# Optimization experiments

Measured on AMD Instinct MI355X. Metric: run time of the kernel, lower is better.

## Reference

```python
import jax, jax.numpy as jnp
from jax import lax
import numpy as np

B, CIN, COUT, H, W = 8, 64, 64, 128, 128
K = 3
KK = K * K  # 9 kernel taps


def setup_inputs() -> dict:
    key = jax.random.key(0)
    ks = jax.random.split(key, 10)
    n = jax.random.normal
    s = 0.05  # keep activations in a sane range
    return {
        "Fi": n(ks[0], (B, CIN, H, W), jnp.float32),
        "Fe": n(ks[1], (B, CIN, H, W), jnp.float32),
        "w1": n(ks[2], (CIN, 2 * CIN, 5, 5), jnp.float32) * s,
        "b1": n(ks[3], (CIN,), jnp.float32) * s,
        "w2": n(ks[4], (CIN, CIN, 3, 3), jnp.float32) * s,
        "b2": n(ks[5], (CIN,), jnp.float32) * s,
        "w_off": n(ks[6], (3 * KK, CIN, 3, 3), jnp.float32) * s,
        "b_off": n(ks[7], (3 * KK,), jnp.float32) * s,
        "w_dcn": n(ks[8], (COUT, CIN, 3, 3), jnp.float32) * s,
        "b_dcn": n(ks[9], (COUT,), jnp.float32) * s,
    }


def _conv(x, w, b, pad):
    y = lax.conv_general_dilated(x, w, (1, 1), [(pad, pad), (pad, pad)],
                                 dimension_numbers=('NCHW', 'OIHW', 'NCHW'))
    return y + b[None, :, None, None]


def _leaky(x):
    return jnp.where(x >= 0, x, 0.1 * x)  # LeakyReLU(0.1)


def _bilinear(img, y, x):
    # img [B,C,H,W]; y, x [B,KK,H,W] fractional sampling coords; zero padding OOB
    Bn, C, Hi, Wi = img.shape
    y0 = jnp.floor(y)
    x0 = jnp.floor(x)
    flat = img.reshape(Bn, C, Hi * Wi)
    out = jnp.zeros((Bn, C) + y.shape[1:], img.dtype)
    for dy, dx in ((0, 0), (0, 1), (1, 0), (1, 1)):
        yi = y0 + dy
        xi = x0 + dx
        wgt = (1.0 - jnp.abs(y - yi)) * (1.0 - jnp.abs(x - xi))
        valid = (yi >= 0) & (yi <= Hi - 1) & (xi >= 0) & (xi <= Wi - 1)
        yc = jnp.clip(yi, 0, Hi - 1).astype(jnp.int32)
        xc = jnp.clip(xi, 0, Wi - 1).astype(jnp.int32)
        idx = (yc * Wi + xc).reshape(Bn, 1, -1)
        v = jnp.take_along_axis(flat, jnp.broadcast_to(idx, (Bn, C, idx.shape[-1])), axis=2)
        v = v.reshape(Bn, C, *y.shape[1:])  # [B,C,KK,H,W]
        out = out + v * (wgt * valid)[:, None]
    return out


def _dcn(x, feat, w_off, b_off, w, b):
    # modulated deformable conv (DCNv2), k=3, stride=1, pad=1, dilation=1
    oo = _conv(feat, w_off, b_off, 1)                 # [B, 3*KK, H, W]
    o1, o2, m = jnp.split(oo, 3, axis=1)              # dy, dx, mask logits
    offset_out = jnp.concatenate([o1, o2], axis=1)
    mask = jax.nn.sigmoid(m)                          # [B,KK,H,W]
    ky, kx = jnp.meshgrid(jnp.arange(K), jnp.arange(K), indexing='ij')
    ky = ky.reshape(KK)
    kx = kx.reshape(KK)
    base_y = (jnp.arange(H)[None, :, None] - 1 + ky[:, None, None]).astype(x.dtype)  # [KK,H,1]
    base_x = (jnp.arange(W)[None, None, :] - 1 + kx[:, None, None]).astype(x.dtype)  # [KK,1,W]
    ys = base_y[None] + o1                            # [B,KK,H,W]
    xs = base_x[None] + o2                            # [B,KK,H,W]
    samp = _bilinear(x, ys, xs) * mask[:, None]       # [B,C,KK,H,W]
    out = jnp.einsum('bckhw,ock->bohw', samp, w.reshape(w.shape[0], w.shape[1], KK))
    return offset_out, out + b[None, :, None, None]


def reference(Fi, Fe, w1, b1, w2, b2, w_off, b_off, w_dcn, b_dcn):
    feat = _leaky(_conv(jnp.concatenate([Fi, Fe], axis=1), w1, b1, 2))
    feat = _leaky(_conv(feat, w2, b2, 1))
    offset_out, aligned = _dcn(Fe, feat, w_off, b_off, w_dcn, b_dcn)
    Ff = jnp.concatenate([Fi, aligned], axis=1)
    return offset_out, Ff
```

## Files before the change

kernel.cpp:

```cpp
#include <hip/hip_runtime.h>
#include <hip/hip_bf16.h>

typedef __bf16 bf16_t;
typedef __attribute__((ext_vector_type(8))) __bf16 bf16x8;
typedef __attribute__((ext_vector_type(4))) float f32x4;

#define Bn 8
#define Hh 128
#define Ww 128
#define HW 16384

#define WP1_B   ((size_t)0)
#define WP2_B   ((size_t)409600)
#define WPO_B   ((size_t)483328)
#define WDCN_B  ((size_t)520192)
#define BIAS_B  ((size_t)667648)
#define XT_B    ((size_t)668672)
#define F1_B    (XT_B + 33554432)
#define F2_B    (F1_B + 16777216)

__global__ void prep_kernel(const float* __restrict__ w1, const float* __restrict__ w2,
                            const float* __restrict__ woff, const float* __restrict__ wdcn,
                            const float* __restrict__ b1, const float* __restrict__ b2,
                            const float* __restrict__ boff, const float* __restrict__ bdcn,
                            char* __restrict__ wsb) {
    bf16_t* wp1 = (bf16_t*)(wsb + WP1_B);
    bf16_t* wp2 = (bf16_t*)(wsb + WP2_B);
    bf16_t* wpo = (bf16_t*)(wsb + WPO_B);
    bf16_t* wd  = (bf16_t*)(wsb + WDCN_B);
    float*  bias= (float*)(wsb + BIAS_B);
    int tid = blockIdx.x * blockDim.x + threadIdx.x;
    int nt  = gridDim.x * blockDim.x;
    for (int i = tid; i < 25*4*4*64*8; i += nt) {
        int j = i & 7, q = i >> 3;
        int n = q % 64; q /= 64;
        int g = q & 3;  q >>= 2;
        int ck = q & 3; int t = q >> 2;
        int cin = ck*32 + g*8 + j;
        wp1[i] = (bf16_t)w1[(n*128 + cin)*25 + t];
    }
    for (int i = tid; i < 9*2*4*64*8; i += nt) {
        int j = i & 7, q = i >> 3;
        int n = q % 64; q /= 64;
        int g = q & 3;  q >>= 2;
        int ck = q & 1; int t = q >> 1;
        int cin = ck*32 + g*8 + j;
        wp2[i] = (bf16_t)w2[(n*64 + cin)*9 + t];
    }
    for (int i = tid; i < 9*2*4*32*8; i += nt) {
        int j = i & 7, q = i >> 3;
        int n = q & 31; q >>= 5;
        int g = q & 3;  q >>= 2;
        int ck = q & 1; int t = q >> 1;
        int cin = ck*32 + g*8 + j;
        wpo[i] = (n < 27) ? (bf16_t)woff[(n*64 + cin)*9 + t] : (bf16_t)0.f;
    }
    for (int i = tid; i < 18*4*4*16*8; i += nt) {
        int j = i & 7, f = i >> 3;
        int l15 = f & 15; f >>= 4;
        int l4  = f & 3;  f >>= 2;
        int ntl = f & 3;  int kc = f >> 2;
        int kg = kc*32 + l4*8 + j;
        int tap = kg >> 6, c = kg & 63;
        int n = ntl*16 + l15;
        wd[i] = (bf16_t)wdcn[n*576 + c*9 + tap];
    }
    if (tid < 64) { bias[tid] = b1[tid]; bias[64+tid] = b2[tid]; bias[160+tid] = bdcn[tid]; }
    if (tid >= 64 && tid < 96) { int n = tid - 64; bias[128+n] = (n < 27) ? boff[n] : 0.f; }
}

__global__ __launch_bounds__(256) void nhwc_kernel(const float* __restrict__ Fi,
                                                   const float* __restrict__ Fe,
                                                   bf16_t* __restrict__ Xt) {
    __shared__ bf16_t tile[64][136];
    const int b  = blockIdx.y;
    const int p0 = blockIdx.x * 64;
    const int px = threadIdx.x & 63;
    const int csub = threadIdx.x >> 6;
    for (int ci = 0; ci < 32; ++ci) {
        int c = csub * 32 + ci;
        const float* src = (c < 64) ? (Fi + (((size_t)(b*64 + c)) << 14))
                                    : (Fe + (((size_t)(b*64 + (c-64))) << 14));
        tile[px][c] = (bf16_t)src[p0 + px];
    }
    __syncthreads();
    const int px2 = threadIdx.x >> 2;
    const int cc  = (threadIdx.x & 3) * 32;
    bf16x8* dst = (bf16x8*)(Xt + ((size_t)(b*HW) + p0 + px2) * 128 + cc);
    const bf16x8* srcl = (const bf16x8*)(&tile[px2][cc]);
    dst[0] = srcl[0]; dst[1] = srcl[1]; dst[2] = srcl[2]; dst[3] = srcl[3];
}

template <int CIN_, int KS, int COUTP, bool LEAKY, bool OUTF32, bool OFFS>
__global__ __launch_bounds__(256) void conv_mfma(const bf16_t* __restrict__ Xt,
                                                 const bf16_t* __restrict__ Wp,
                                                 const float* __restrict__ bias,
                                                 bf16_t* __restrict__ outb,
                                                 float* __restrict__ outf,
                                                 float* __restrict__ out0) {
    constexpr int PAD = KS / 2;
    constexpr int HR  = 4 + KS - 1;
    constexpr int HC  = 64 + KS - 1;
    constexpr int NC  = CIN_ / 32;
    constexpr int NT  = COUTP / 16;
    __shared__ bf16_t stg[HR * HC * 40];

    const int tid  = threadIdx.x;
    const int lane = tid & 63;
    const int wid  = tid >> 6;
    const int b    = blockIdx.z;
    const int h0   = blockIdx.y * 4;
    const int w0   = blockIdx.x * 64;
    const int l15  = lane & 15;
    const int l4   = lane >> 4;

    f32x4 acc[4][NT];
#pragma unroll
    for (int m = 0; m < 4; ++m)
#pragma unroll
        for (int nt = 0; nt < NT; ++nt)
#pragma unroll
            for (int r = 0; r < 4; ++r) acc[m][nt][r] = 0.f;

    const bf16_t Z0 = (bf16_t)0.f;
    const bf16x8 zv = {Z0, Z0, Z0, Z0, Z0, Z0, Z0, Z0};
    const bf16x8* wpt = (const bf16x8*)Wp;

    for (int ck = 0; ck < NC; ++ck) {
        for (int s = tid; s < HR * HC; s += 256) {
            const int srow = s / HC, scol = s % HC;
            const int gh = h0 - PAD + srow, gw = w0 - PAD + scol;
            bf16x8 v0 = zv, v1 = zv, v2 = zv, v3 = zv;
            if (((unsigned)gh < 128u) && ((unsigned)gw < 128u)) {
                const bf16x8* gp = (const bf16x8*)(Xt + (((size_t)(b*HW) + (gh << 7) + gw)) * CIN_ + ck * 32);
                v0 = gp[0]; v1 = gp[1]; v2 = gp[2]; v3 = gp[3];
            }
            bf16x8* ldst = (bf16x8*)(&stg[s * 40]);
            ldst[0] = v0; ldst[1] = v1; ldst[2] = v2; ldst[3] = v3;
        }
        __syncthreads();
        int t = 0;
#pragma unroll
        for (int dy = 0; dy < KS; ++dy) {
#pragma unroll
            for (int dx = 0; dx < KS; ++dx, ++t) {
                bf16x8 a[4];
#pragma unroll
                for (int m = 0; m < 4; ++m)
                    a[m] = *(const bf16x8*)(&stg[((wid + dy) * HC + (m * 16 + l15 + dx)) * 40 + l4 * 8]);
                bf16x8 bb[NT];
#pragma unroll
                for (int nt = 0; nt < NT; ++nt)
                    bb[nt] = wpt[((size_t)((t * NC + ck) * 4 + l4)) * COUTP + nt * 16 + l15];
#pragma unroll
                for (int m = 0; m < 4; ++m)
#pragma unroll
                    for (int nt = 0; nt < NT; ++nt)
                        acc[m][nt] = __builtin_amdgcn_mfma_f32_16x16x32_bf16(a[m], bb[nt], acc[m][nt], 0, 0, 0);
            }
        }
        __syncthreads();
    }

    const int hrow = h0 + wid;
#pragma unroll
    for (int m = 0; m < 4; ++m) {
#pragma unroll
        for (int nt = 0; nt < NT; ++nt) {
            const int n = nt * 16 + l15;
            const float bs = bias[n];
#pragma unroll
            for (int r = 0; r < 4; ++r) {
                const int px = w0 + m * 16 + l4 * 4 + r;
                float v = acc[m][nt][r] + bs;
                if (LEAKY) v = (v >= 0.f) ? v : 0.1f * v;
                const size_t pix = (size_t)(hrow << 7) + px;
                if (OUTF32) outf[(((size_t)(b * COUTP + n)) << 14) + pix] = v;
                else        outb[(((size_t)(b * HW)) + pix) * COUTP + n] = (bf16_t)v;
                if (OFFS) {
                    if (n < 18) out0[(((size_t)(b * 18 + n)) << 14) + pix] = v;
                }
            }
        }
    }
}

__global__ void copy_fi(const float* __restrict__ Fi, float* __restrict__ out1) {
    const int b = blockIdx.y;
    const int i = blockIdx.x * blockDim.x + threadIdx.x;
    const int e = i << 2;
    const int c = e >> 14;
    const int p = e & 16383;
    const float4* src = reinterpret_cast<const float4*>(Fi);
    float4* dst = reinterpret_cast<float4*>(out1);
    size_t se = ((size_t)b << 20) + e;
    size_t de = (((size_t)(b * 128 + c)) << 14) + p;
    dst[de >> 2] = src[se >> 2];
}

__global__ __launch_bounds__(512) void dcn_mfma(const bf16_t* __restrict__ Xt,
                                                const float* __restrict__ OO,
                                                const bf16_t* __restrict__ Wd,
                                                const float* __restrict__ bias,
                                                float* __restrict__ out1) {
    __shared__ bf16_t Bs[10 * 4 * 4 * 16 * 8];

    const int tid  = threadIdx.x;
    const int lane = tid & 63;
    const int wave = tid >> 6;
    const int l15  = lane & 15;
    const int l4   = lane >> 4;
    const int b    = blockIdx.y;
    const int p0   = blockIdx.x * 256 + wave * 32;

    f32x4 acc[2][4];
#pragma unroll
    for (int nt = 0; nt < 4; ++nt) {
        const float bs = bias[nt * 16 + l15];
#pragma unroll
        for (int a = 0; a < 2; ++a) { acc[a][nt][0] = bs; acc[a][nt][1] = bs; acc[a][nt][2] = bs; acc[a][nt][3] = bs; }
    }

    const bf16_t* feb = Xt + ((size_t)(b * HW)) * 128 + 64;
    const bf16x8* Bsv = (const bf16x8*)Bs;
    const bf16x8* Wdv = (const bf16x8*)Wd;

#pragma unroll
    for (int phase = 0; phase < 2; ++phase) {
        const int fbase = phase * 2560;
        const int fcnt  = phase ? 2048 : 2560;
        bf16x8* Bsw = (bf16x8*)Bs;
        for (int f = tid; f < fcnt; f += 512) Bsw[f] = Wdv[fbase + f];
        __syncthreads();

        const int t0 = phase ? 5 : 0;
        const int t1 = phase ? 9 : 5;
        for (int k = t0; k < t1; ++k) {
            const int ky = k / 3, kx = k % 3;
#pragma unroll
            for (int a = 0; a < 2; ++a) {
                const int p  = p0 + a * 16 + l15;
                const int h  = p >> 7, w = p & 127;
                const float o1v = OO[(((size_t)(b * 32 + k)) << 14) + p];
                const float o2v = OO[(((size_t)(b * 32 + 9 + k)) << 14) + p];
                const float ml  = OO[(((size_t)(b * 32 + 18 + k)) << 14) + p];
                const float m = 1.f / (1.f + __expf(-ml));

                const float y = (float)(h - 1 + ky) + o1v;
                const float x = (float)(w - 1 + kx) + o2v;
                const float y0f = floorf(y), x0f = floorf(x);
                const float fy = y - y0f, fx = x - x0f;
                const int y0 = (int)y0f, x0 = (int)x0f;

                const bool vy0 = (unsigned)y0 < 128u;
                const bool vy1 = (unsigned)(y0 + 1) < 128u;
                const bool vx0 = (unsigned)x0 < 128u;
                const bool vx1 = (unsigned)(x0 + 1) < 128u;

                const int y0c = min(max(y0, 0), 127);
                const int y1c = min(max(y0 + 1, 0), 127);
                const int x0c = min(max(x0, 0), 127);
                const int x1c = min(max(x0 + 1, 0), 127);

                float w00 = (1.f - fy) * (1.f - fx) * m; w00 = (vy0 && vx0) ? w00 : 0.f;
                float w01 = (1.f - fy) * fx * m;         w01 = (vy0 && vx1) ? w01 : 0.f;
                float w10 = fy * (1.f - fx) * m;         w10 = (vy1 && vx0) ? w10 : 0.f;
                float w11 = fy * fx * m;                 w11 = (vy1 && vx1) ? w11 : 0.f;

                const bf16_t* p00 = feb + ((size_t)((y0c << 7) + x0c)) * 128;
                const bf16_t* p01 = feb + ((size_t)((y0c << 7) + x1c)) * 128;
                const bf16_t* p10 = feb + ((size_t)((y1c << 7) + x0c)) * 128;
                const bf16_t* p11 = feb + ((size_t)((y1c << 7) + x1c)) * 128;

#pragma unroll
                for (int cc = 0; cc < 2; ++cc) {
                    const int c0 = cc * 32 + l4 * 8;
                    const bf16x8 v00 = *(const bf16x8*)(p00 + c0);
                    const bf16x8 v01 = *(const bf16x8*)(p01 + c0);
                    const bf16x8 v10 = *(const bf16x8*)(p10 + c0);
                    const bf16x8 v11 = *(const bf16x8*)(p11 + c0);
                    bf16x8 af;
#pragma unroll
                    for (int j = 0; j < 8; ++j) {
                        af[j] = (bf16_t)(w00 * (float)v00[j] + w01 * (float)v01[j]
                                       + w10 * (float)v10[j] + w11 * (float)v11[j]);
                    }
                    const int kcl = (k * 2 + cc) - phase * 10;
#pragma unroll
                    for (int nt = 0; nt < 4; ++nt) {
                        const bf16x8 bf = Bsv[((kcl * 4 + nt) * 4 + l4) * 16 + l15];
                        acc[a][nt] = __builtin_amdgcn_mfma_f32_16x16x32_bf16(af, bf, acc[a][nt], 0, 0, 0);
                    }
                }
            }
        }
        __syncthreads();
    }

#pragma unroll
    for (int a = 0; a < 2; ++a) {
#pragma unroll
        for (int nt = 0; nt < 4; ++nt) {
            const int o = nt * 16 + l15;
#pragma unroll
            for (int r = 0; r < 4; ++r) {
                const int p = p0 + a * 16 + l4 * 4 + r;
                out1[(((size_t)(b * 128 + 64 + o)) << 14) + p] = acc[a][nt][r];
            }
        }
    }
}

extern "C" void kernel_launch(void* const* d_in, const int* in_sizes, int n_in,
                              void* d_out, int out_size, void* d_ws, size_t ws_size,
                              hipStream_t stream) {
    const float* Fi    = (const float*)d_in[0];
    const float* Fe    = (const float*)d_in[1];
    const float* w1    = (const float*)d_in[2];
    const float* b1    = (const float*)d_in[3];
    const float* w2    = (const float*)d_in[4];
    const float* b2    = (const float*)d_in[5];
    const float* w_off = (const float*)d_in[6];
    const float* b_off = (const float*)d_in[7];
    const float* w_dcn = (const float*)d_in[8];
    const float* b_dcn = (const float*)d_in[9];

    char* wsb = (char*)d_ws;
    bf16_t* wp1   = (bf16_t*)(wsb + WP1_B);
    bf16_t* wp2   = (bf16_t*)(wsb + WP2_B);
    bf16_t* wpo   = (bf16_t*)(wsb + WPO_B);
    bf16_t* wdcnf = (bf16_t*)(wsb + WDCN_B);
    float*  bias  = (float*)(wsb + BIAS_B);
    bf16_t* Xt    = (bf16_t*)(wsb + XT_B);
    bf16_t* feat1 = (bf16_t*)(wsb + F1_B);
    bf16_t* feat2 = (bf16_t*)(wsb + F2_B);
    float*  OO    = (float*)(wsb + F1_B);

    float* out0 = (float*)d_out;
    float* out1 = out0 + (size_t)Bn * 18 * HW;

    prep_kernel<<<256, 256, 0, stream>>>(w1, w2, w_off, w_dcn, b1, b2, b_off, b_dcn, wsb);

    nhwc_kernel<<<dim3(256, 8), 256, 0, stream>>>(Fi, Fe, Xt);

    conv_mfma<128, 5, 64, true, false, false>
        <<<dim3(2, 32, 8), 256, 0, stream>>>(Xt, wp1, bias, feat1, nullptr, nullptr);

    conv_mfma<64, 3, 64, true, false, false>
        <<<dim3(2, 32, 8), 256, 0, stream>>>(feat1, wp2, bias + 64, feat2, nullptr, nullptr);

    conv_mfma<64, 3, 32, false, true, true>
        <<<dim3(2, 32, 8), 256, 0, stream>>>(feat2, wpo, bias + 128, nullptr, OO, out0);

    copy_fi<<<dim3(1024, 8), 256, 0, stream>>>(Fi, out1);

    dcn_mfma<<<dim3(64, 8), 512, 0, stream>>>(Xt, OO, wdcnf, bias + 160, out1);
}
```

Before: 327.5 us.

## Shrink DCN blocks, drop LDS weight staging, read weights from global

The deformable-conv kernel now gives each wave 16 pixels instead of 32 and launches four times as many 256-thread blocks. The two-phase LDS staging of the DCN weights and its barriers are gone; B fragments are loaded straight from global memory (L1/L2-cached) inside a fully unrolled 9-tap loop. The aim is more waves in flight to hide the latency of the scattered bilinear gathers, and no sync stalls. In exchange, weight fetches are repeated per wave through the cache and there is less reuse per loaded weight.

New measurement: 462.6 us. 1.41x slower.

```diff
diff --git a/kernel.cpp b/kernel.cpp
--- a/kernel.cpp
+++ b/kernel.cpp
@@ -198,115 +198,96 @@
     dst[de >> 2] = src[se >> 2];
 }
 
-__global__ __launch_bounds__(512) void dcn_mfma(const bf16_t* __restrict__ Xt,
-                                                const float* __restrict__ OO,
-                                                const bf16_t* __restrict__ Wd,
-                                                const float* __restrict__ bias,
-                                                float* __restrict__ out1) {
-    __shared__ bf16_t Bs[10 * 4 * 4 * 16 * 8];
-
+__global__ __launch_bounds__(256, 8) void dcn_mfma(const bf16_t* __restrict__ Xt,
+                                                   const float* __restrict__ OO,
+                                                   const bf16_t* __restrict__ Wd,
+                                                   const float* __restrict__ bias,
+                                                   float* __restrict__ out1) {
     const int tid  = threadIdx.x;
     const int lane = tid & 63;
     const int wave = tid >> 6;
     const int l15  = lane & 15;
     const int l4   = lane >> 4;
     const int b    = blockIdx.y;
-    const int p0   = blockIdx.x * 256 + wave * 32;
-
-    f32x4 acc[2][4];
+    const int p0   = blockIdx.x * 64 + wave * 16;
+
+    f32x4 acc[4];
 #pragma unroll
     for (int nt = 0; nt < 4; ++nt) {
         const float bs = bias[nt * 16 + l15];
-#pragma unroll
-        for (int a = 0; a < 2; ++a) { acc[a][nt][0] = bs; acc[a][nt][1] = bs; acc[a][nt][2] = bs; acc[a][nt][3] = bs; }
+        acc[nt][0] = bs; acc[nt][1] = bs; acc[nt][2] = bs; acc[nt][3] = bs;
     }
 
     const bf16_t* feb = Xt + ((size_t)(b * HW)) * 128 + 64;
-    const bf16x8* Bsv = (const bf16x8*)Bs;
     const bf16x8* Wdv = (const bf16x8*)Wd;
 
-#pragma unroll
-    for (int phase = 0; phase < 2; ++phase) {
-        const int fbase = phase * 2560;
-        const int fcnt  = phase ? 2048 : 2560;
-        bf16x8* Bsw = (bf16x8*)Bs;
-        for (int f = tid; f < fcnt; f += 512) Bsw[f] = Wdv[fbase + f];
-        __syncthreads();
-
-        const int t0 = phase ? 5 : 0;
-        const int t1 = phase ? 9 : 5;
-        for (int k = t0; k < t1; ++k) {
-            const int ky = k / 3, kx = k % 3;
-#pragma unroll
-            for (int a = 0; a < 2; ++a) {
-                const int p  = p0 + a * 16 + l15;
-                const int h  = p >> 7, w = p & 127;
-                const float o1v = OO[(((size_t)(b * 32 + k)) << 14) + p];
-                const float o2v = OO[(((size_t)(b * 32 + 9 + k)) << 14) + p];
-                const float ml  = OO[(((size_t)(b * 32 + 18 + k)) << 14) + p];
-                const float m = 1.f / (1.f + __expf(-ml));
-
-                const float y = (float)(h - 1 + ky) + o1v;
-                const float x = (float)(w - 1 + kx) + o2v;
-                const float y0f = floorf(y), x0f = floorf(x);
-                const float fy = y - y0f, fx = x - x0f;
-                const int y0 = (int)y0f, x0 = (int)x0f;
-
-                const bool vy0 = (unsigned)y0 < 128u;
-                const bool vy1 = (unsigned)(y0 + 1) < 128u;
-                const bool vx0 = (unsigned)x0 < 128u;
-                const bool vx1 = (unsigned)(x0 + 1) < 128u;
-
-                const int y0c = min(max(y0, 0), 127);
-                const int y1c = min(max(y0 + 1, 0), 127);
-                const int x0c = min(max(x0, 0), 127);
-                const int x1c = min(max(x0 + 1, 0), 127);
-
-                float w00 = (1.f - fy) * (1.f - fx) * m; w00 = (vy0 && vx0) ? w00 : 0.f;
-                float w01 = (1.f - fy) * fx * m;         w01 = (vy0 && vx1) ? w01 : 0.f;
-                float w10 = fy * (1.f - fx) * m;         w10 = (vy1 && vx0) ? w10 : 0.f;
-                float w11 = fy * fx * m;                 w11 = (vy1 && vx1) ? w11 : 0.f;
-
-                const bf16_t* p00 = feb + ((size_t)((y0c << 7) + x0c)) * 128;
-                const bf16_t* p01 = feb + ((size_t)((y0c << 7) + x1c)) * 128;
-                const bf16_t* p10 = feb + ((size_t)((y1c << 7) + x0c)) * 128;
-                const bf16_t* p11 = feb + ((size_t)((y1c << 7) + x1c)) * 128;
-
-#pragma unroll
-                for (int cc = 0; cc < 2; ++cc) {
-                    const int c0 = cc * 32 + l4 * 8;
-                    const bf16x8 v00 = *(const bf16x8*)(p00 + c0);
-                    const bf16x8 v01 = *(const bf16x8*)(p01 + c0);
-                    const bf16x8 v10 = *(const bf16x8*)(p10 + c0);
-                    const bf16x8 v11 = *(const bf16x8*)(p11 + c0);
-                    bf16x8 af;
-#pragma unroll
-                    for (int j = 0; j < 8; ++j) {
-                        af[j] = (bf16_t)(w00 * (float)v00[j] + w01 * (float)v01[j]
-                                       + w10 * (float)v10[j] + w11 * (float)v11[j]);
-                    }
-                    const int kcl = (k * 2 + cc) - phase * 10;
-#pragma unroll
-                    for (int nt = 0; nt < 4; ++nt) {
-                        const bf16x8 bf = Bsv[((kcl * 4 + nt) * 4 + l4) * 16 + l15];
-                        acc[a][nt] = __builtin_amdgcn_mfma_f32_16x16x32_bf16(af, bf, acc[a][nt], 0, 0, 0);
-                    }
-                }
-            }
-        }
-        __syncthreads();
-    }
-
-#pragma unroll
-    for (int a = 0; a < 2; ++a) {
-#pragma unroll
-        for (int nt = 0; nt < 4; ++nt) {
-            const int o = nt * 16 + l15;
-#pragma unroll
-            for (int r = 0; r < 4; ++r) {
-                const int p = p0 + a * 16 + l4 * 4 + r;
-                out1[(((size_t)(b * 128 + 64 + o)) << 14) + p] = acc[a][nt][r];
-            }
+    const int p = p0 + l15;
+    const int h = p >> 7, w = p & 127;
+    const size_t oobase = (((size_t)(b * 32)) << 14) + p;
+
+#pragma unroll
+    for (int k = 0; k < 9; ++k) {
+        const int ky = k / 3, kx = k % 3;
+        const float o1v = OO[oobase + ((size_t)k << 14)];
+        const float o2v = OO[oobase + ((size_t)(9 + k) << 14)];
+        const float ml  = OO[oobase + ((size_t)(18 + k) << 14)];
+        const float m = 1.f / (1.f + __expf(-ml));
+
+        const float y = (float)(h - 1 + ky) + o1v;
+        const float x = (float)(w - 1 + kx) + o2v;
+        const float y0f = floorf(y), x0f = floorf(x);
+        const float fy = y - y0f, fx = x - x0f;
+        const int y0 = (int)y0f, x0 = (int)x0f;
+
+        const bool vy0 = (unsigned)y0 < 128u;
+        const bool vy1 = (unsigned)(y0 + 1) < 128u;
+        const bool vx0 = (unsigned)x0 < 128u;
+        const bool vx1 = (unsigned)(x0 + 1) < 128u;
+
+        const int y0c = min(max(y0, 0), 127);
+        const int y1c = min(max(y0 + 1, 0), 127);
+        const int x0c = min(max(x0, 0), 127);
+        const int x1c = min(max(x0 + 1, 0), 127);
+
+        float w00 = (1.f - fy) * (1.f - fx) * m; w00 = (vy0 && vx0) ? w00 : 0.f;
+        float w01 = (1.f - fy) * fx * m;         w01 = (vy0 && vx1) ? w01 : 0.f;
+        float w10 = fy * (1.f - fx) * m;         w10 = (vy1 && vx0) ? w10 : 0.f;
+        float w11 = fy * fx * m;                 w11 = (vy1 && vx1) ? w11 : 0.f;
+
+        const bf16_t* p00 = feb + ((size_t)((y0c << 7) + x0c)) * 128;
+        const bf16_t* p01 = feb + ((size_t)((y0c << 7) + x1c)) * 128;
+        const bf16_t* p10 = feb + ((size_t)((y1c << 7) + x0c)) * 128;
+        const bf16_t* p11 = feb + ((size_t)((y1c << 7) + x1c)) * 128;
+
+#pragma unroll
+        for (int cc = 0; cc < 2; ++cc) {
+            const int c0 = cc * 32 + l4 * 8;
+            const bf16x8 v00 = *(const bf16x8*)(p00 + c0);
+            const bf16x8 v01 = *(const bf16x8*)(p01 + c0);
+            const bf16x8 v10 = *(const bf16x8*)(p10 + c0);
+            const bf16x8 v11 = *(const bf16x8*)(p11 + c0);
+            bf16x8 af;
+#pragma unroll
+            for (int j = 0; j < 8; ++j) {
+                af[j] = (bf16_t)(w00 * (float)v00[j] + w01 * (float)v01[j]
+                               + w10 * (float)v10[j] + w11 * (float)v11[j]);
+            }
+            const int kc = k * 2 + cc;
+#pragma unroll
+            for (int nt = 0; nt < 4; ++nt) {
+                const bf16x8 bf = Wdv[((kc * 4 + nt) * 4 + l4) * 16 + l15];
+                acc[nt] = __builtin_amdgcn_mfma_f32_16x16x32_bf16(af, bf, acc[nt], 0, 0, 0);
+            }
+        }
+    }
+
+#pragma unroll
+    for (int nt = 0; nt < 4; ++nt) {
+        const int o = nt * 16 + l15;
+#pragma unroll
+        for (int r = 0; r < 4; ++r) {
+            const int px = p0 + l4 * 4 + r;
+            out1[(((size_t)(b * 128 + 64 + o)) << 14) + px] = acc[nt][r];
         }
     }
 }
@@ -354,5 +335,5 @@
 
     copy_fi<<<dim3(1024, 8), 256, 0, stream>>>(Fi, out1);
 
-    dcn_mfma<<<dim3(64, 8), 512, 0, stream>>>(Xt, OO, wdcnf, bias + 160, out1);
-}
+    dcn_mfma<<<dim3(256, 8), 256, 0, stream>>>(Xt, OO, wdcnf, bias + 160, out1);
+}
```
